# Optimization experiments

Hardware: AMD Instinct MI355X
Metric: run time of the kernel (lower is better)

## Reference

```python
import jax, jax.numpy as jnp
import numpy as np

B, T, N, F = 4, 24, 1024, 96
H, HD = 3, 32      # spatial GATConv: 3 heads, head-dim 32 (averaged -> 32 per branch, 3 branches -> 96)
GH, GHD = 4, 24    # GroupedGAT: 4 heads concatenated -> 96
E = 8192           # edges per graph


def setup_inputs() -> dict:
    key = jax.random.key(0)
    ks = jax.random.split(key, 24)
    s_in = 1.0 / np.sqrt(F)
    def gat_params(k):
        k1, k2, k3, k4 = jax.random.split(k, 4)
        return (jax.random.normal(k1, (F, H * HD), jnp.float32) * s_in,
                jax.random.normal(k2, (H, HD), jnp.float32) * 0.1,
                jax.random.normal(k3, (H, HD), jnp.float32) * 0.1,
                jax.random.normal(k4, (H, HD), jnp.float32) * 0.02)
    W_d, al_d, ar_d, b_d = gat_params(ks[3])
    W_m, al_m, ar_m, b_m = gat_params(ks[4])
    W_s, al_s, ar_s, b_s = gat_params(ks[5])
    inp = {
        "input": jax.random.normal(ks[0], (B, T, N, F), jnp.float32),
        "spatial_embedding": jax.random.normal(ks[1], (B, T, N, F), jnp.float32),
        "temporal_embedding": jax.random.normal(ks[2], (B, T, N, F), jnp.float32),
        "src_d": jax.random.randint(ks[6], (E,), 0, N, jnp.int32),
        "dst_d": (jnp.arange(E) % N).astype(jnp.int32),
        "src_m": jax.random.randint(ks[7], (E,), 0, N, jnp.int32),
        "dst_m": (jnp.arange(E) % N).astype(jnp.int32),
        "src_s": jax.random.randint(ks[8], (E,), 0, N, jnp.int32),
        "dst_s": (jnp.arange(E) % N).astype(jnp.int32),
        "W_d": W_d, "al_d": al_d, "ar_d": ar_d, "b_d": b_d,
        "W_m": W_m, "al_m": al_m, "ar_m": ar_m, "b_m": b_m,
        "W_s": W_s, "al_s": al_s, "ar_s": ar_s, "b_s": b_s,
        "Wg": jax.random.normal(ks[9], (F, GH * GHD), jnp.float32) * s_in,
        "agl": jax.random.normal(ks[10], (GH, GHD), jnp.float32) * 0.1,
        "agr": jax.random.normal(ks[11], (GH, GHD), jnp.float32) * 0.1,
        "Wf": jax.random.normal(ks[12], (2 * F, F), jnp.float32) * (1.0 / np.sqrt(2 * F)),
        "bf": jnp.zeros((F,), jnp.float32),
    }
    return inp


def _gat(x, src, dst, W, al, ar, b):
    # x: (N, K, F) node features with K = T*B batched feature slots
    K = x.shape[1]
    h = (x @ W).reshape(N, K, H, HD)                       # (N,K,H,HD)
    el = (h * al).sum(-1)                                  # (N,K,H)
    er = (h * ar).sum(-1)
    e = jax.nn.leaky_relu(el[src] + er[dst], 0.2)          # (E,K,H)
    emax = jax.ops.segment_max(e, dst, num_segments=N)
    emax = jnp.where(jnp.isfinite(emax), emax, 0.0)
    ex = jnp.exp(e - emax[dst])
    denom = jax.ops.segment_sum(ex, dst, num_segments=N)
    alpha = ex / (denom[dst] + 1e-9)                       # edge softmax over incoming edges
    out = jax.ops.segment_sum(h[src] * alpha[..., None], dst, num_segments=N)
    return (out + b).mean(2)                               # average heads -> (N,K,HD)


def reference(input, spatial_embedding, temporal_embedding,
              src_d, dst_d, src_m, dst_m, src_s, dst_s,
              W_d, al_d, ar_d, b_d, W_m, al_m, ar_m, b_m, W_s, al_s, ar_s, b_s,
              Wg, agl, agr, Wf, bf):
    # ---------------- SpatialBlock ----------------
    residual_s = input                                     # input_dim == output_dim
    x_in = input + spatial_embedding
    # torch: input.transpose(0,2).reshape(N,-1,F) -> slot order is (t,b)
    x = jnp.transpose(x_in, (2, 1, 0, 3)).reshape(N, T * B, F)
    xd = _gat(x, src_d, dst_d, W_d, al_d, ar_d, b_d)
    xm = _gat(x, src_m, dst_m, W_m, al_m, ar_m, b_m)
    xs = _gat(x, src_s, dst_s, W_s, al_s, ar_s, b_s)
    x_attn = jnp.concatenate([xd, xm, xs], axis=-1)        # (N, T*B, 3*HD=F)
    # torch: transpose(0,1).reshape(batch,T,N,-1)  (keeps original (t,b) slot order quirk)
    x_attn = jnp.transpose(x_attn, (1, 0, 2)).reshape(B, T, N, F)
    cov0 = spatial_embedding[:, 0]                         # (B,N,F)
    attn_S = jax.nn.softmax(cov0 @ jnp.swapaxes(cov0, 1, 2), axis=2)  # (B,N,N)
    # NOTE: embedding_x branch in SpatialBlock is dead code (out is overwritten); skipped.
    spatial = residual_s + x_attn

    # ---------------- TemporalBlock ----------------
    residual_t = input
    xt = jnp.swapaxes(input, 1, 2).reshape(B * N, T, F)    # (B*N, T, F), index k=b*N+n
    # GroupedGAT: dense multi-head GAT over the T=period_num time steps
    hg = (xt @ Wg).reshape(B * N, T, GH, GHD)
    elg = (hg * agl).sum(-1)                               # (BN,T,GH)
    erg = (hg * agr).sum(-1)
    eg = jax.nn.leaky_relu(elg[:, :, None, :] + erg[:, None, :, :], 0.2)  # (BN,Ti,Tj,GH)
    alphag = jax.nn.softmax(eg, axis=2)
    xg = jnp.einsum('kijh,kjhd->kihd', alphag, hg).reshape(B * N, T, GH * GHD)
    covT = temporal_embedding[:, :, 0]                     # (B,T,F)
    attn_T = jax.nn.softmax(covT @ jnp.swapaxes(covT, 1, 2), axis=1)      # softmax over dim=1 as in torch
    # torch: attn.repeat(N,1,1) paired with x of batch index b*N+n -> uses attn[(b*N+n) % B]
    idx = (jnp.arange(B * N) % B)
    emb = jnp.einsum('kij,kjf->kif', attn_T[idx], xt)      # (BN,T,F)
    xg = xg * jax.nn.sigmoid(emb)
    xg = jnp.swapaxes(xg.reshape(B, N, T, F), 1, 2)        # (B,T,N,F)
    temporal = residual_t + xg

    # ---------------- Fusion ----------------
    z = jax.nn.sigmoid(jnp.concatenate([spatial, temporal], axis=-1) @ Wf + bf)
    out = z * spatial + (1.0 - z) * temporal + input
    return out, attn_S
```

## Files before the change

kernel.cpp:

```cpp
#include <hip/hip_runtime.h>
#include <hip/hip_bf16.h>

typedef long long i64;
typedef __attribute__((ext_vector_type(8))) short short8b;
typedef __attribute__((ext_vector_type(4))) short short4b;
typedef __attribute__((ext_vector_type(4))) float f32x4;

union U8 { short8b v; ushort s[8]; };
union U4 { short4b v; ushort s[4]; };

static __device__ __forceinline__ float bs2f(ushort u) {
    union { unsigned int i; float f; } x; x.i = ((unsigned int)u) << 16; return x.f;
}
static __device__ __forceinline__ ushort f2bs(float f) {
    __hip_bfloat16 h = __float2bfloat16(f);
    return *reinterpret_cast<ushort*>(&h);
}
static __device__ __forceinline__ void mfma_bf16(f32x4& acc, short8b a, short8b b) {
    asm volatile("v_mfma_f32_16x16x32_bf16 %0, %1, %2, %0" : "+v"(acc) : "v"(a), "v"(b));
}
static __device__ __forceinline__ void mfma_fence() {
    asm volatile("s_nop 7\n\ts_nop 7\n\ts_nop 7");
}


__global__ __launch_bounds__(256) void prep_weights_kernel(
        const float* __restrict__ Wd, const float* __restrict__ Wm,
        const float* __restrict__ Ws, const float* __restrict__ Wg,
        const float* __restrict__ Wf,
        const float* __restrict__ ald, const float* __restrict__ ard,
        const float* __restrict__ alm, const float* __restrict__ arm,
        const float* __restrict__ als, const float* __restrict__ ars,
        const float* __restrict__ agl, const float* __restrict__ agr,
        ushort* __restrict__ wtab) {
    int idx = blockIdx.x * 256 + threadIdx.x;
    if (idx >= 61440) return;
    if (idx < 43008) {
        int w = idx / 10752, rem = idx - w * 10752;
        int c = rem / 96, k = rem - c * 96;
        float v;
        if (w < 3) {
            const float* W = (w == 0) ? Wd : (w == 1) ? Wm : Ws;
            if (c < 96) {
                v = W[k * 96 + c];
            } else {
                int j = c - 96, h = j >> 1;
                const float* a = (j & 1) ? ((w == 0) ? ard : (w == 1) ? arm : ars)
                                         : ((w == 0) ? ald : (w == 1) ? alm : als);
                v = 0.f;
                for (int d = 0; d < 32; ++d) v += W[k * 96 + h * 32 + d] * a[h * 32 + d];
            }
        } else {
            if (c < 96) {
                v = Wg[k * 96 + c];
            } else {
                int j = c - 96, g = j & 3;
                const float* a = (j >> 2) ? agr : agl;
                v = 0.f;
                for (int d = 0; d < 24; ++d) v += Wg[k * 96 + g * 24 + d] * a[g * 24 + d];
            }
        }
        wtab[w * 10752 + c * 96 + k] = f2bs(v);
    } else {
        int rem = idx - 43008;
        int c = rem / 192, k = rem - c * 192;
        wtab[43008 + c * 192 + k] = f2bs(Wf[k * 96 + c]);
    }
}

__global__ __launch_bounds__(256) void build_x_kernel(const float* __restrict__ inp,
                                                      const float* __restrict__ spat,
                                                      ushort* __restrict__ x) {
    int i4 = blockIdx.x * 256 + threadIdx.x;
    int q = i4 % 24;
    int r = i4 / 24;
    int n = r & 1023, bt = r >> 10;
    int t = bt % 24, b = bt / 24;
    int k = t * 4 + b;
    float4 a = ((const float4*)inp)[i4];
    float4 s = ((const float4*)spat)[i4];
    U4 u;
    u.s[0] = f2bs(a.x + s.x); u.s[1] = f2bs(a.y + s.y);
    u.s[2] = f2bs(a.z + s.z); u.s[3] = f2bs(a.w + s.w);
    *(short4b*)&x[((i64)((k << 10) | n)) * 96 + q * 4] = u.v;
}

__global__ __launch_bounds__(256) void gemm96_mfma_kernel(const ushort* __restrict__ X,
                                                          const ushort* __restrict__ wt,
                                                          ushort* __restrict__ Ho,
                                                          float* __restrict__ el,
                                                          float* __restrict__ er) {
    __shared__ ushort Xs[128 * 104];
    __shared__ ushort Wt[112 * 104];
    int tid = threadIdx.x;
    i64 row0 = (i64)blockIdx.x * 128;
    for (int i = tid; i < 1344; i += 256) {
        int c = i / 12, kg = i - c * 12;
        *(short8b*)&Wt[c * 104 + kg * 8] = *(const short8b*)&wt[c * 96 + kg * 8];
    }
    for (int i = tid; i < 1536; i += 256) {
        int r = i / 12, q = i - r * 12;
        *(short8b*)&Xs[r * 104 + q * 8] = *(const short8b*)&X[(row0 + r) * 96 + q * 8];
    }
    __syncthreads();
    int wid = tid >> 6, lane = tid & 63;
    int lr = lane & 15, lk = lane >> 4;
    f32x4 acc[2][7];
#pragma unroll
    for (int m = 0; m < 2; ++m)
#pragma unroll
        for (int c = 0; c < 7; ++c) acc[m][c] = (f32x4){0.f, 0.f, 0.f, 0.f};
    const ushort* xa = &Xs[(wid * 32 + lr) * 104 + lk * 8];
    const ushort* wb = &Wt[lr * 104 + lk * 8];
#pragma unroll
    for (int ks = 0; ks < 3; ++ks) {
        short8b a0 = *(const short8b*)(xa + ks * 32);
        short8b a1 = *(const short8b*)(xa + 16 * 104 + ks * 32);
#pragma unroll
        for (int c = 0; c < 7; ++c) {
            short8b b = *(const short8b*)(wb + c * 16 * 104 + ks * 32);
            mfma_bf16(acc[0][c], a0, b);
            mfma_bf16(acc[1][c], a1, b);
        }
    }
    mfma_fence();
#pragma unroll
    for (int m = 0; m < 2; ++m) {
#pragma unroll
        for (int c = 0; c < 6; ++c)
#pragma unroll
            for (int r = 0; r < 4; ++r) {
                i64 row = row0 + wid * 32 + m * 16 + lk * 4 + r;
                Ho[row * 96 + c * 16 + lr] = f2bs(acc[m][c][r]);
            }
        if (lr < 6) {
            float* dst = (lr & 1) ? er : el;
            int h = lr >> 1;
#pragma unroll
            for (int r = 0; r < 4; ++r) {
                i64 row = row0 + wid * 32 + m * 16 + lk * 4 + r;
                dst[row * 4 + h] = acc[m][6][r];
            }
        }
    }
}

__global__ __launch_bounds__(256) void gemm96_hg_mfma_kernel(const float* __restrict__ inp,
                                                             const ushort* __restrict__ wt,
                                                             ushort* __restrict__ Ho,
                                                             float* __restrict__ elg,
                                                             float* __restrict__ erg) {
    __shared__ ushort Xs[128 * 104];
    __shared__ ushort Wt[112 * 104];
    int tid = threadIdx.x;
    i64 row0 = (i64)blockIdx.x * 128;
    for (int i = tid; i < 1344; i += 256) {
        int c = i / 12, kg = i - c * 12;
        *(short8b*)&Wt[c * 104 + kg * 8] = *(const short8b*)&wt[c * 96 + kg * 8];
    }
    for (int i = tid; i < 3072; i += 256) {
        int r = i / 24, q = i - r * 24;
        int row = (int)row0 + r;
        int kk = row / 24, t = row - kk * 24;
        int b = kk >> 10, n = kk & 1023;
        float4 v = ((const float4*)inp)[((i64)(((b * 24 + t) << 10) | n)) * 24 + q];
        U4 u;
        u.s[0] = f2bs(v.x); u.s[1] = f2bs(v.y); u.s[2] = f2bs(v.z); u.s[3] = f2bs(v.w);
        *(short4b*)&Xs[r * 104 + q * 4] = u.v;
    }
    __syncthreads();
    int wid = tid >> 6, lane = tid & 63;
    int lr = lane & 15, lk = lane >> 4;
    f32x4 acc[2][7];
#pragma unroll
    for (int m = 0; m < 2; ++m)
#pragma unroll
        for (int c = 0; c < 7; ++c) acc[m][c] = (f32x4){0.f, 0.f, 0.f, 0.f};
    const ushort* xa = &Xs[(wid * 32 + lr) * 104 + lk * 8];
    const ushort* wb = &Wt[lr * 104 + lk * 8];
#pragma unroll
    for (int ks = 0; ks < 3; ++ks) {
        short8b a0 = *(const short8b*)(xa + ks * 32);
        short8b a1 = *(const short8b*)(xa + 16 * 104 + ks * 32);
#pragma unroll
        for (int c = 0; c < 7; ++c) {
            short8b b = *(const short8b*)(wb + c * 16 * 104 + ks * 32);
            mfma_bf16(acc[0][c], a0, b);
            mfma_bf16(acc[1][c], a1, b);
        }
    }
    mfma_fence();
#pragma unroll
    for (int m = 0; m < 2; ++m) {
#pragma unroll
        for (int c = 0; c < 6; ++c)
#pragma unroll
            for (int r = 0; r < 4; ++r) {
                i64 row = row0 + wid * 32 + m * 16 + lk * 4 + r;
                Ho[row * 96 + c * 16 + lr] = f2bs(acc[m][c][r]);
            }
        if (lr < 8) {
            float* dst = (lr >> 2) ? erg : elg;
            int g = lr & 3;
#pragma unroll
            for (int r = 0; r < 4; ++r) {
                i64 row = row0 + wid * 32 + m * 16 + lk * 4 + r;
                dst[row * 4 + g] = acc[m][6][r];
            }
        }
    }
}

__global__ __launch_bounds__(256) void gat_agg_kernel(const ushort* __restrict__ H2,
                                                      const float* __restrict__ el,
                                                      const float* __restrict__ er,
                                                      const int* __restrict__ src,
                                                      const float* __restrict__ bv,
                                                      ushort* __restrict__ xattn,
                                                      int g) {
    int tid = threadIdx.x;
    int pp = tid >> 3, l8 = tid & 7;
    int p = blockIdx.x * 32 + pp;
    int k = p >> 10, n = p & 1023;
    int d0 = l8 * 4;
    i64 kb = (i64)(k << 10);
    int s_own = src[n + l8 * 1024];
    float4 elv = *(const float4*)&el[(kb | s_own) * 4];
    float4 erv = *(const float4*)&er[(kb | n) * 4];
    float e[3], m[3];
    {
        float ev0 = elv.x + erv.x, ev1 = elv.y + erv.y, ev2 = elv.z + erv.z;
        e[0] = ev0 >= 0.f ? ev0 : 0.2f * ev0;
        e[1] = ev1 >= 0.f ? ev1 : 0.2f * ev1;
        e[2] = ev2 >= 0.f ? ev2 : 0.2f * ev2;
        m[0] = e[0]; m[1] = e[1]; m[2] = e[2];
    }
#pragma unroll
    for (int mask = 1; mask < 8; mask <<= 1) {
#pragma unroll
        for (int h = 0; h < 3; ++h) m[h] = fmaxf(m[h], __shfl_xor(m[h], mask, 8));
    }
    float pex[3], S[3];
#pragma unroll
    for (int h = 0; h < 3; ++h) { pex[h] = expf(e[h] - m[h]); S[h] = pex[h]; }
#pragma unroll
    for (int mask = 1; mask < 8; mask <<= 1) {
#pragma unroll
        for (int h = 0; h < 3; ++h) S[h] += __shfl_xor(S[h], mask, 8);
    }
    float w[3];
#pragma unroll
    for (int h = 0; h < 3; ++h) w[h] = pex[h] / (S[h] + 1e-9f);
    float acc[4] = {0.f, 0.f, 0.f, 0.f};
#pragma unroll
    for (int j = 0; j < 8; ++j) {
        int sj = __shfl(s_own, j, 8);
        float a0 = __shfl(w[0], j, 8);
        float a1 = __shfl(w[1], j, 8);
        float a2 = __shfl(w[2], j, 8);
        const ushort* hp = &H2[(kb | sj) * 96 + d0];
        U4 h0, h1, h2;
        h0.v = *(const short4b*)&hp[0];
        h1.v = *(const short4b*)&hp[32];
        h2.v = *(const short4b*)&hp[64];
#pragma unroll
        for (int c = 0; c < 4; ++c)
            acc[c] += a0 * bs2f(h0.s[c]) + a1 * bs2f(h1.s[c]) + a2 * bs2f(h2.s[c]);
    }
    float4 b0 = *(const float4*)&bv[d0];
    float4 b1 = *(const float4*)&bv[32 + d0];
    float4 b2 = *(const float4*)&bv[64 + d0];
    float bsum[4] = {b0.x + b1.x + b2.x, b0.y + b1.y + b2.y,
                     b0.z + b1.z + b2.z, b0.w + b1.w + b2.w};
    U4 u;
#pragma unroll
    for (int c = 0; c < 4; ++c) u.s[c] = f2bs((acc[c] + bsum[c]) * (1.f / 3.f));
    *(short4b*)&xattn[(kb | n) * 96 + g * 32 + d0] = u.v;
}

__global__ __launch_bounds__(256) void attn_scores_kernel(const float* __restrict__ spat,
                                                          float* __restrict__ attnS) {
    extern __shared__ __align__(16) float dynf[];
    float* As = dynf;
    float* Bs = dynf + 12800;
    int bid = blockIdx.x;
    int b = bid >> 7;
    int it = (bid >> 4) & 7;
    int jt = bid & 15;
    int i0 = it * 128, j0 = jt * 64;
    const float* C = spat + (i64)b * 24 * 1024 * 96;
    int tid = threadIdx.x;
    float4* As4 = (float4*)As;
    float4* Bs4 = (float4*)Bs;
    const float4* Ai = (const float4*)(C + (i64)i0 * 96);
    const float4* Bj = (const float4*)(C + (i64)j0 * 96);
    for (int i = tid; i < 3072; i += 256) {
        int row = i / 24, q = i - row * 24;
        As4[row * 25 + q] = Ai[i];
    }
    for (int i = tid; i < 1536; i += 256) {
        int row = i / 24, q = i - row * 24;
        Bs4[row * 25 + q] = Bj[i];
    }
    __syncthreads();
    int tj = tid & 15, ti = tid >> 4;
    float acc[8][4];
#pragma unroll
    for (int r = 0; r < 8; ++r)
#pragma unroll
        for (int s = 0; s < 4; ++s) acc[r][s] = 0.f;
    for (int k4 = 0; k4 < 24; ++k4) {
        float4 a[8], bv[4];
#pragma unroll
        for (int r = 0; r < 8; ++r) a[r] = As4[(ti * 8 + r) * 25 + k4];
#pragma unroll
        for (int s = 0; s < 4; ++s) bv[s] = Bs4[(s * 16 + tj) * 25 + k4];
#pragma unroll
        for (int r = 0; r < 8; ++r)
#pragma unroll
            for (int s = 0; s < 4; ++s)
                acc[r][s] += a[r].x * bv[s].x + a[r].y * bv[s].y + a[r].z * bv[s].z + a[r].w * bv[s].w;
    }
#pragma unroll
    for (int r = 0; r < 8; ++r) {
        i64 orow = ((i64)(b << 10) + i0 + ti * 8 + r) * 1024 + j0;
#pragma unroll
        for (int s = 0; s < 4; ++s) attnS[orow + s * 16 + tj] = acc[r][s];
    }
}

__global__ __launch_bounds__(256) void attn_softmax_kernel(float* __restrict__ attnS) {
    i64 base = (i64)blockIdx.x * 1024;
    float4* row4 = (float4*)(attnS + base);
    int tid = threadIdx.x;
    float4 v = row4[tid];
    __shared__ float red[256];
    float m = fmaxf(fmaxf(v.x, v.y), fmaxf(v.z, v.w));
    red[tid] = m;
    __syncthreads();
    for (int st = 128; st > 0; st >>= 1) {
        if (tid < st) red[tid] = fmaxf(red[tid], red[tid + st]);
        __syncthreads();
    }
    m = red[0];
    __syncthreads();
    v.x = expf(v.x - m); v.y = expf(v.y - m); v.z = expf(v.z - m); v.w = expf(v.w - m);
    red[tid] = v.x + v.y + v.z + v.w;
    __syncthreads();
    for (int st = 128; st > 0; st >>= 1) {
        if (tid < st) red[tid] += red[tid + st];
        __syncthreads();
    }
    float inv = 1.f / red[0];
    v.x *= inv; v.y *= inv; v.z *= inv; v.w *= inv;
    row4[tid] = v;
}

__global__ __launch_bounds__(576) void attn_t_kernel(const float* __restrict__ temp,
                                                     float* __restrict__ attnT) {
    int b = blockIdx.x;
    int tid = threadIdx.x;
    __shared__ float cs[24][96];
    __shared__ float M[24][24];
    for (int i = tid; i < 2304; i += 576) {
        int r = i / 96, f = i - r * 96;
        cs[r][f] = temp[((i64)(b * 24 + r)) * 1024 * 96 + f];
    }
    __syncthreads();
    int i = tid / 24, j = tid - i * 24;
    float s = 0.f;
#pragma unroll
    for (int f = 0; f < 96; ++f) s += cs[i][f] * cs[j][f];
    M[i][j] = s;
    __syncthreads();
    float m = -1e30f;
#pragma unroll
    for (int i2 = 0; i2 < 24; ++i2) m = fmaxf(m, M[i2][j]);
    float sum = 0.f;
#pragma unroll
    for (int i2 = 0; i2 < 24; ++i2) sum += expf(M[i2][j] - m);
    attnT[((i64)b * 24 + i) * 24 + j] = expf(M[i][j] - m) / sum;
}

__global__ __launch_bounds__(576) void sig_kernel(const float* __restrict__ inp,
                                                  const float* __restrict__ attnT,
                                                  ushort* __restrict__ sig) {
    int kk = blockIdx.x;
    int b = kk >> 10, n = kk & 1023;
    __shared__ __align__(16) float xs[24 * 100];
    __shared__ float ats[576];
    int tid = threadIdx.x;
    {
        int r = tid / 24, q = tid - (tid / 24) * 24;
        *(float4*)&xs[r * 100 + q * 4] =
            ((const float4*)inp)[(((i64)(b * 24 + r)) << 10 | n) * 24 + q];
        ats[tid] = attnT[(kk & 3) * 576 + tid];
    }
    __syncthreads();
    int i = tid / 24, f4 = tid - (tid / 24) * 24;
    const float* ap = &ats[i * 24];
    float4 acc = {0.f, 0.f, 0.f, 0.f};
#pragma unroll
    for (int j = 0; j < 24; ++j) {
        float a = ap[j];
        float4 v = *(const float4*)&xs[j * 100 + f4 * 4];
        acc.x += a * v.x; acc.y += a * v.y; acc.z += a * v.z; acc.w += a * v.w;
    }
    U4 o;
    o.s[0] = f2bs(1.f / (1.f + expf(-acc.x)));
    o.s[1] = f2bs(1.f / (1.f + expf(-acc.y)));
    o.s[2] = f2bs(1.f / (1.f + expf(-acc.z)));
    o.s[3] = f2bs(1.f / (1.f + expf(-acc.w)));
    *(short4b*)&sig[(i64)kk * 2304 + i * 96 + f4 * 4] = o.v;
}

__global__ __launch_bounds__(192) void xg_kernel(const ushort* __restrict__ hg,
                                                 const float* __restrict__ elgb,
                                                 const float* __restrict__ ergb,
                                                 const ushort* __restrict__ sig,
                                                 ushort* __restrict__ gated) {
    int kk = blockIdx.x;
    __shared__ __align__(16) ushort hgs[24 * 96];
    __shared__ __align__(16) float alphaT[4 * 24 * 32];
    __shared__ __align__(16) float elg[24][4], erg[24][4];
    int tid = threadIdx.x;
    for (int i = tid; i < 576; i += 192)
        *(short4b*)&hgs[i * 4] = *(const short4b*)&hg[(i64)kk * 2304 + i * 4];
    for (int i = tid; i < 48; i += 192) {
        int r = i >> 1;
        if (i & 1) *(float4*)&erg[r][0] = ((const float4*)ergb)[(i64)kk * 24 + r];
        else       *(float4*)&elg[r][0] = ((const float4*)elgb)[(i64)kk * 24 + r];
    }
    __syncthreads();
    {
        int i = tid >> 3, g = (tid >> 1) & 3, half = tid & 1;
        int j0 = half * 12;
        float eli = elg[i][g];
        float ev[12];
        float m = -1e30f;
#pragma unroll
        for (int j = 0; j < 12; ++j) {
            float e = eli + erg[j0 + j][g];
            e = e >= 0.f ? e : 0.2f * e;
            ev[j] = e;
            m = fmaxf(m, e);
        }
        m = fmaxf(m, __shfl_xor(m, 1));
        float sum = 0.f;
#pragma unroll
        for (int j = 0; j < 12; ++j) { ev[j] = expf(ev[j] - m); sum += ev[j]; }
        sum += __shfl_xor(sum, 1);
        float inv = 1.f / sum;
        int slot = ((i / 3) * 4 + (i - (i / 3) * 3)) ^ (g << 3);
#pragma unroll
        for (int j = 0; j < 12; ++j) alphaT[g * 768 + (j0 + j) * 32 + slot] = ev[j] * inv;
    }
    __syncthreads();
    int ig = tid / 24, f4 = tid - (tid / 24) * 24;
    int g = f4 / 6;
    float4 xg0 = {0,0,0,0}, xg1 = {0,0,0,0}, xg2 = {0,0,0,0};
    const float* aT = &alphaT[g * 768 + ((ig * 4) ^ (g << 3))];
#pragma unroll
    for (int j = 0; j < 24; ++j) {
        U4 uh; uh.v = *(const short4b*)&hgs[j * 96 + f4 * 4];
        float4 a4 = *(const float4*)&aT[j * 32];
        float h0 = bs2f(uh.s[0]), h1 = bs2f(uh.s[1]), h2 = bs2f(uh.s[2]), h3 = bs2f(uh.s[3]);
        xg0.x += a4.x * h0; xg0.y += a4.x * h1; xg0.z += a4.x * h2; xg0.w += a4.x * h3;
        xg1.x += a4.y * h0; xg1.y += a4.y * h1; xg1.z += a4.y * h2; xg1.w += a4.y * h3;
        xg2.x += a4.z * h0; xg2.y += a4.z * h1; xg2.z += a4.z * h2; xg2.w += a4.z * h3;
    }
    i64 obase = (i64)kk * 2304 + f4 * 4;
#pragma unroll
    for (int r = 0; r < 3; ++r) {
        float4 xg = (r == 0) ? xg0 : (r == 1) ? xg1 : xg2;
        i64 off = obase + (i64)(ig * 3 + r) * 96;
        U4 us; us.v = *(const short4b*)&sig[off];
        U4 o;
        o.s[0] = f2bs(xg.x * bs2f(us.s[0]));
        o.s[1] = f2bs(xg.y * bs2f(us.s[1]));
        o.s[2] = f2bs(xg.z * bs2f(us.s[2]));
        o.s[3] = f2bs(xg.w * bs2f(us.s[3]));
        *(short4b*)&gated[off] = o.v;
    }
}

__global__ __launch_bounds__(384) void fusion_mfma_kernel(const float* __restrict__ inp,
                                                          const ushort* __restrict__ xattn,
                                                          const ushort* __restrict__ gated,
                                                          const ushort* __restrict__ wtf,
                                                          const float* __restrict__ bfv,
                                                          float* __restrict__ outb) {
    extern __shared__ __align__(16) ushort dynlds[];
    ushort* Xs = dynlds;
    ushort* Wt = dynlds + 96 * 200;
    float* zbuf = (float*)Wt;
    int tid = threadIdx.x;
    i64 row0 = (i64)blockIdx.x * 96;
    for (int i = tid; i < 2304; i += 384) {
        int c = i / 24, kg = i - c * 24;
        *(short8b*)&Wt[c * 200 + kg * 8] = *(const short8b*)&wtf[c * 192 + kg * 8];
    }
    for (int i = tid; i < 1152; i += 384) {
        int r = i / 12, q = i - r * 12;
        i64 grow = row0 + r;
        int n = (int)(grow & 1023);
        int bt = (int)(grow >> 10);
        int t = bt % 24, b = bt / 24;
        float4 iv0 = ((const float4*)inp)[grow * 24 + q * 2];
        float4 iv1 = ((const float4*)inp)[grow * 24 + q * 2 + 1];
        U8 xa; xa.v = *(const short8b*)&xattn[grow * 96 + q * 8];
        U8 gd; gd.v = *(const short8b*)&gated[(((i64)((b << 10) | n)) * 24 + t) * 96 + q * 8];
        float ivf[8] = {iv0.x, iv0.y, iv0.z, iv0.w, iv1.x, iv1.y, iv1.z, iv1.w};
        U8 sp, tm;
#pragma unroll
        for (int j = 0; j < 8; ++j) {
            sp.s[j] = f2bs(ivf[j] + bs2f(xa.s[j]));
            tm.s[j] = f2bs(ivf[j] + bs2f(gd.s[j]));
        }
        *(short8b*)&Xs[r * 200 + q * 8] = sp.v;
        *(short8b*)&Xs[r * 200 + 96 + q * 8] = tm.v;
    }
    __syncthreads();
    int wid = tid >> 6, lane = tid & 63;
    int lr = lane & 15, lk = lane >> 4;
    f32x4 acc[6];
#pragma unroll
    for (int c = 0; c < 6; ++c) acc[c] = (f32x4){0.f, 0.f, 0.f, 0.f};
    const ushort* xa = &Xs[(wid * 16 + lr) * 200 + lk * 8];
    const ushort* wb = &Wt[lr * 200 + lk * 8];
#pragma unroll
    for (int ks = 0; ks < 6; ++ks) {
        short8b a = *(const short8b*)(xa + ks * 32);
#pragma unroll
        for (int c = 0; c < 6; ++c) {
            short8b b = *(const short8b*)(wb + c * 16 * 200 + ks * 32);
            mfma_bf16(acc[c], a, b);
        }
    }
    mfma_fence();
    float4 ivp[6];
#pragma unroll
    for (int ii = 0; ii < 6; ++ii) {
        int i = tid + ii * 384;
        int r2 = i / 24, q = i - r2 * 24;
        ivp[ii] = ((const float4*)inp)[(row0 + r2) * 24 + q];
    }
    __syncthreads();
#pragma unroll
    for (int c = 0; c < 6; ++c) {
        int col = c * 16 + lr;
        float bfc = bfv[col];
#pragma unroll
        for (int r = 0; r < 4; ++r) {
            int lrow = wid * 16 + lk * 4 + r;
            zbuf[lrow * 100 + col] = 1.f / (1.f + expf(-(acc[c][r] + bfc)));
        }
    }
    __syncthreads();
#pragma unroll
    for (int ii = 0; ii < 6; ++ii) {
        int i = tid + ii * 384;
        int r2 = i / 24, q = i - r2 * 24;
        i64 grow = row0 + r2;
        float4 iv = ivp[ii];
        float4 zv = *(const float4*)&zbuf[r2 * 100 + q * 4];
        U4 spv; spv.v = *(const short4b*)&Xs[r2 * 200 + q * 4];
        U4 tmv; tmv.v = *(const short4b*)&Xs[r2 * 200 + 96 + q * 4];
        float4 o;
        o.x = zv.x * bs2f(spv.s[0]) + (1.f - zv.x) * bs2f(tmv.s[0]) + iv.x;
        o.y = zv.y * bs2f(spv.s[1]) + (1.f - zv.y) * bs2f(tmv.s[1]) + iv.y;
        o.z = zv.z * bs2f(spv.s[2]) + (1.f - zv.z) * bs2f(tmv.s[2]) + iv.z;
        o.w = zv.w * bs2f(spv.s[3]) + (1.f - zv.w) * bs2f(tmv.s[3]) + iv.w;
        ((float4*)outb)[grow * 24 + q] = o;
    }
}

extern "C" void kernel_launch(void* const* d_in, const int* in_sizes, int n_in,
                              void* d_out, int out_size, void* d_ws, size_t ws_size,
                              hipStream_t stream) {
    const float* input = (const float*)d_in[0];
    const float* spat  = (const float*)d_in[1];
    const float* temp  = (const float*)d_in[2];
    const int* src_d = (const int*)d_in[3];
    const int* src_m = (const int*)d_in[5];
    const int* src_s = (const int*)d_in[7];
    const float* W_d  = (const float*)d_in[9];
    const float* al_d = (const float*)d_in[10];
    const float* ar_d = (const float*)d_in[11];
    const float* b_d  = (const float*)d_in[12];
    const float* W_m  = (const float*)d_in[13];
    const float* al_m = (const float*)d_in[14];
    const float* ar_m = (const float*)d_in[15];
    const float* b_m  = (const float*)d_in[16];
    const float* W_s  = (const float*)d_in[17];
    const float* al_s = (const float*)d_in[18];
    const float* ar_s = (const float*)d_in[19];
    const float* b_s  = (const float*)d_in[20];
    const float* Wg   = (const float*)d_in[21];
    const float* agl  = (const float*)d_in[22];
    const float* agr  = (const float*)d_in[23];
    const float* Wf   = (const float*)d_in[24];
    const float* bf_  = (const float*)d_in[25];

    float* outb  = (float*)d_out;
    float* attnS = outb + 9437184;

    float* wsf = (float*)d_ws;
    ushort* xbf      = (ushort*)wsf;
    ushort* hgbf     = xbf;
    ushort* H2bf     = (ushort*)(wsf + 4718592);
    ushort* gatedbf  = H2bf;
    ushort* xattnbf  = (ushort*)(wsf + 9437184);
    float* el    = wsf + 14155776;
    float* er    = wsf + 14548992;
    float* elgb  = el;
    float* ergb  = er;
    ushort* wtab = (ushort*)(wsf + 14942208);
    ushort* wt_d = wtab;
    ushort* wt_m = wtab + 10752;
    ushort* wt_s = wtab + 21504;
    ushort* wtg  = wtab + 32256;
    ushort* wtf  = wtab + 43008;
    float* attnT = wsf + 14972928;
    ushort* sigbf = (ushort*)outb;

    static int attr_set = 0;
    if (!attr_set) {
        hipFuncSetAttribute((const void*)fusion_mfma_kernel,
                            hipFuncAttributeMaxDynamicSharedMemorySize, 76800);
        hipFuncSetAttribute((const void*)attn_scores_kernel,
                            hipFuncAttributeMaxDynamicSharedMemorySize, 76800);
        attr_set = 1;
    }

    prep_weights_kernel<<<240, 256, 0, stream>>>(W_d, W_m, W_s, Wg, Wf,
                                                 al_d, ar_d, al_m, ar_m, al_s, ar_s,
                                                 agl, agr, wtab);
    build_x_kernel<<<9216, 256, 0, stream>>>(input, spat, xbf);

    const ushort* Wgat[3] = {wt_d, wt_m, wt_s};
    const float* bgat[3] = {b_d, b_m, b_s};
    const int* srcs[3] = {src_d, src_m, src_s};
    for (int g = 0; g < 3; ++g) {
        gemm96_mfma_kernel<<<768, 256, 0, stream>>>(xbf, Wgat[g], H2bf, el, er);
        gat_agg_kernel<<<3072, 256, 0, stream>>>(H2bf, el, er, srcs[g], bgat[g],
                                                 xattnbf, g);
    }

    attn_scores_kernel<<<512, 256, 76800, stream>>>(spat, attnS);
    attn_softmax_kernel<<<4096, 256, 0, stream>>>(attnS);

    attn_t_kernel<<<4, 576, 0, stream>>>(temp, attnT);
    sig_kernel<<<4096, 576, 0, stream>>>(input, attnT, sigbf);
    gemm96_hg_mfma_kernel<<<768, 256, 0, stream>>>(input, wtg, hgbf, elgb, ergb);
    xg_kernel<<<4096, 192, 0, stream>>>(hgbf, elgb, ergb, sigbf, gatedbf);
    fusion_mfma_kernel<<<1024, 384, 76800, stream>>>(input, xattnbf, gatedbf, wtf,
                                                     bf_, outb);
}
```

Measured before the change: 251.7 us.

## Fuse build_x into GAT GEMMs and merge sigmoid gate into xg kernel

Removes the build_x kernel: each of the three spatial GEMM launches now reads input and spatial_embedding in fp32, adds them and converts to bf16 while staging its tile in shared memory. The sig and xg kernels become a single 576-thread kernel that computes the temporal-attention sigmoid gate in registers, so the bf16 sig buffer no longer makes a round trip through memory. The fusion kernel also stops prefetching the input residual into registers before the matmul and instead loads it in the epilogue. The trade-off is that the input+spatial add and conversion is now redone in each of the three GEMM launches, which read fp32 data twice per launch.

```diff
diff --git a/kernel.cpp b/kernel.cpp
--- a/kernel.cpp
+++ b/kernel.cpp
@@ -68,24 +68,8 @@
     }
 }
 
-__global__ __launch_bounds__(256) void build_x_kernel(const float* __restrict__ inp,
-                                                      const float* __restrict__ spat,
-                                                      ushort* __restrict__ x) {
-    int i4 = blockIdx.x * 256 + threadIdx.x;
-    int q = i4 % 24;
-    int r = i4 / 24;
-    int n = r & 1023, bt = r >> 10;
-    int t = bt % 24, b = bt / 24;
-    int k = t * 4 + b;
-    float4 a = ((const float4*)inp)[i4];
-    float4 s = ((const float4*)spat)[i4];
-    U4 u;
-    u.s[0] = f2bs(a.x + s.x); u.s[1] = f2bs(a.y + s.y);
-    u.s[2] = f2bs(a.z + s.z); u.s[3] = f2bs(a.w + s.w);
-    *(short4b*)&x[((i64)((k << 10) | n)) * 96 + q * 4] = u.v;
-}
-
-__global__ __launch_bounds__(256) void gemm96_mfma_kernel(const ushort* __restrict__ X,
+__global__ __launch_bounds__(256) void gemm96_mfma_kernel(const float* __restrict__ inp,
+                                                          const float* __restrict__ spat,
                                                           const ushort* __restrict__ wt,
                                                           ushort* __restrict__ Ho,
                                                           float* __restrict__ el,
@@ -98,9 +82,18 @@
         int c = i / 12, kg = i - c * 12;
         *(short8b*)&Wt[c * 104 + kg * 8] = *(const short8b*)&wt[c * 96 + kg * 8];
     }
-    for (int i = tid; i < 1536; i += 256) {
-        int r = i / 12, q = i - r * 12;
-        *(short8b*)&Xs[r * 104 + q * 8] = *(const short8b*)&X[(row0 + r) * 96 + q * 8];
+    for (int i = tid; i < 3072; i += 256) {
+        int r = i / 24, q = i - r * 24;
+        int row = (int)row0 + r;
+        int k = row >> 10, n = row & 1023;
+        int bb = k & 3, t = k >> 2;
+        i64 base = ((i64)(((bb * 24 + t) << 10) | n)) * 24 + q;
+        float4 a = ((const float4*)inp)[base];
+        float4 s = ((const float4*)spat)[base];
+        U4 u;
+        u.s[0] = f2bs(a.x + s.x); u.s[1] = f2bs(a.y + s.y);
+        u.s[2] = f2bs(a.z + s.z); u.s[3] = f2bs(a.w + s.w);
+        *(short4b*)&Xs[r * 104 + q * 4] = u.v;
     }
     __syncthreads();
     int wid = tid >> 6, lane = tid & 63;
@@ -382,57 +375,32 @@
     attnT[((i64)b * 24 + i) * 24 + j] = expf(M[i][j] - m) / sum;
 }
 
-__global__ __launch_bounds__(576) void sig_kernel(const float* __restrict__ inp,
-                                                  const float* __restrict__ attnT,
-                                                  ushort* __restrict__ sig) {
+__global__ __launch_bounds__(576) void sigxg_kernel(const float* __restrict__ inp,
+                                                    const float* __restrict__ attnT,
+                                                    const ushort* __restrict__ hg,
+                                                    const float* __restrict__ elgb,
+                                                    const float* __restrict__ ergb,
+                                                    ushort* __restrict__ gated) {
     int kk = blockIdx.x;
     int b = kk >> 10, n = kk & 1023;
     __shared__ __align__(16) float xs[24 * 100];
     __shared__ float ats[576];
-    int tid = threadIdx.x;
-    {
-        int r = tid / 24, q = tid - (tid / 24) * 24;
-        *(float4*)&xs[r * 100 + q * 4] =
-            ((const float4*)inp)[(((i64)(b * 24 + r)) << 10 | n) * 24 + q];
-        ats[tid] = attnT[(kk & 3) * 576 + tid];
-    }
-    __syncthreads();
-    int i = tid / 24, f4 = tid - (tid / 24) * 24;
-    const float* ap = &ats[i * 24];
-    float4 acc = {0.f, 0.f, 0.f, 0.f};
-#pragma unroll
-    for (int j = 0; j < 24; ++j) {
-        float a = ap[j];
-        float4 v = *(const float4*)&xs[j * 100 + f4 * 4];
-        acc.x += a * v.x; acc.y += a * v.y; acc.z += a * v.z; acc.w += a * v.w;
-    }
-    U4 o;
-    o.s[0] = f2bs(1.f / (1.f + expf(-acc.x)));
-    o.s[1] = f2bs(1.f / (1.f + expf(-acc.y)));
-    o.s[2] = f2bs(1.f / (1.f + expf(-acc.z)));
-    o.s[3] = f2bs(1.f / (1.f + expf(-acc.w)));
-    *(short4b*)&sig[(i64)kk * 2304 + i * 96 + f4 * 4] = o.v;
-}
-
-__global__ __launch_bounds__(192) void xg_kernel(const ushort* __restrict__ hg,
-                                                 const float* __restrict__ elgb,
-                                                 const float* __restrict__ ergb,
-                                                 const ushort* __restrict__ sig,
-                                                 ushort* __restrict__ gated) {
-    int kk = blockIdx.x;
     __shared__ __align__(16) ushort hgs[24 * 96];
     __shared__ __align__(16) float alphaT[4 * 24 * 32];
     __shared__ __align__(16) float elg[24][4], erg[24][4];
     int tid = threadIdx.x;
-    for (int i = tid; i < 576; i += 192)
-        *(short4b*)&hgs[i * 4] = *(const short4b*)&hg[(i64)kk * 2304 + i * 4];
-    for (int i = tid; i < 48; i += 192) {
-        int r = i >> 1;
-        if (i & 1) *(float4*)&erg[r][0] = ((const float4*)ergb)[(i64)kk * 24 + r];
-        else       *(float4*)&elg[r][0] = ((const float4*)elgb)[(i64)kk * 24 + r];
-    }
-    __syncthreads();
-    {
+    int r = tid / 24, q = tid - r * 24;
+    ((float4*)xs)[r * 25 + q] =
+        ((const float4*)inp)[(((i64)(b * 24 + r)) << 10 | n) * 24 + q];
+    ats[tid] = attnT[(kk & 3) * 576 + tid];
+    *(short4b*)&hgs[tid * 4] = *(const short4b*)&hg[(i64)kk * 2304 + tid * 4];
+    if (tid < 48) {
+        int rr = tid >> 1;
+        if (tid & 1) *(float4*)&erg[rr][0] = ((const float4*)ergb)[(i64)kk * 24 + rr];
+        else         *(float4*)&elg[rr][0] = ((const float4*)elgb)[(i64)kk * 24 + rr];
+    }
+    __syncthreads();
+    if (tid < 192) {
         int i = tid >> 3, g = (tid >> 1) & 3, half = tid & 1;
         int j0 = half * 12;
         float eli = elg[i][g];
@@ -455,33 +423,38 @@
 #pragma unroll
         for (int j = 0; j < 12; ++j) alphaT[g * 768 + (j0 + j) * 32 + slot] = ev[j] * inv;
     }
-    __syncthreads();
-    int ig = tid / 24, f4 = tid - (tid / 24) * 24;
-    int g = f4 / 6;
-    float4 xg0 = {0,0,0,0}, xg1 = {0,0,0,0}, xg2 = {0,0,0,0};
-    const float* aT = &alphaT[g * 768 + ((ig * 4) ^ (g << 3))];
+    float4 emb = {0.f, 0.f, 0.f, 0.f};
+    {
+        const float* ap = &ats[r * 24];
+#pragma unroll
+        for (int j = 0; j < 24; ++j) {
+            float a = ap[j];
+            float4 v = *(const float4*)&xs[j * 100 + q * 4];
+            emb.x += a * v.x; emb.y += a * v.y; emb.z += a * v.z; emb.w += a * v.w;
+        }
+    }
+    float sg0 = 1.f / (1.f + expf(-emb.x));
+    float sg1 = 1.f / (1.f + expf(-emb.y));
+    float sg2 = 1.f / (1.f + expf(-emb.z));
+    float sg3 = 1.f / (1.f + expf(-emb.w));
+    __syncthreads();
+    int g = q / 6;
+    int slot = ((r / 3) * 4 + (r - (r / 3) * 3)) ^ (g << 3);
+    const float* aT = &alphaT[g * 768 + slot];
+    float4 xg = {0.f, 0.f, 0.f, 0.f};
 #pragma unroll
     for (int j = 0; j < 24; ++j) {
-        U4 uh; uh.v = *(const short4b*)&hgs[j * 96 + f4 * 4];
-        float4 a4 = *(const float4*)&aT[j * 32];
-        float h0 = bs2f(uh.s[0]), h1 = bs2f(uh.s[1]), h2 = bs2f(uh.s[2]), h3 = bs2f(uh.s[3]);
-        xg0.x += a4.x * h0; xg0.y += a4.x * h1; xg0.z += a4.x * h2; xg0.w += a4.x * h3;
-        xg1.x += a4.y * h0; xg1.y += a4.y * h1; xg1.z += a4.y * h2; xg1.w += a4.y * h3;
-        xg2.x += a4.z * h0; xg2.y += a4.z * h1; xg2.z += a4.z * h2; xg2.w += a4.z * h3;
-    }
-    i64 obase = (i64)kk * 2304 + f4 * 4;
-#pragma unroll
-    for (int r = 0; r < 3; ++r) {
-        float4 xg = (r == 0) ? xg0 : (r == 1) ? xg1 : xg2;
-        i64 off = obase + (i64)(ig * 3 + r) * 96;
-        U4 us; us.v = *(const short4b*)&sig[off];
-        U4 o;
-        o.s[0] = f2bs(xg.x * bs2f(us.s[0]));
-        o.s[1] = f2bs(xg.y * bs2f(us.s[1]));
-        o.s[2] = f2bs(xg.z * bs2f(us.s[2]));
-        o.s[3] = f2bs(xg.w * bs2f(us.s[3]));
-        *(short4b*)&gated[off] = o.v;
-    }
+        float a = aT[j * 32];
+        U4 uh; uh.v = *(const short4b*)&hgs[j * 96 + q * 4];
+        xg.x += a * bs2f(uh.s[0]); xg.y += a * bs2f(uh.s[1]);
+        xg.z += a * bs2f(uh.s[2]); xg.w += a * bs2f(uh.s[3]);
+    }
+    U4 o;
+    o.s[0] = f2bs(xg.x * sg0);
+    o.s[1] = f2bs(xg.y * sg1);
+    o.s[2] = f2bs(xg.z * sg2);
+    o.s[3] = f2bs(xg.w * sg3);
+    *(short4b*)&gated[(i64)kk * 2304 + r * 96 + q * 4] = o.v;
 }
 
 __global__ __launch_bounds__(384) void fusion_mfma_kernel(const float* __restrict__ inp,
@@ -538,13 +511,6 @@
         }
     }
     mfma_fence();
-    float4 ivp[6];
-#pragma unroll
-    for (int ii = 0; ii < 6; ++ii) {
-        int i = tid + ii * 384;
-        int r2 = i / 24, q = i - r2 * 24;
-        ivp[ii] = ((const float4*)inp)[(row0 + r2) * 24 + q];
-    }
     __syncthreads();
 #pragma unroll
     for (int c = 0; c < 6; ++c) {
@@ -557,12 +523,10 @@
         }
     }
     __syncthreads();
-#pragma unroll
-    for (int ii = 0; ii < 6; ++ii) {
-        int i = tid + ii * 384;
+    for (int i = tid; i < 2304; i += 384) {
         int r2 = i / 24, q = i - r2 * 24;
         i64 grow = row0 + r2;
-        float4 iv = ivp[ii];
+        float4 iv = ((const float4*)inp)[grow * 24 + q];
         float4 zv = *(const float4*)&zbuf[r2 * 100 + q * 4];
         U4 spv; spv.v = *(const short4b*)&Xs[r2 * 200 + q * 4];
         U4 tmv; tmv.v = *(const short4b*)&Xs[r2 * 200 + 96 + q * 4];
@@ -606,8 +570,7 @@
     float* attnS = outb + 9437184;
 
     float* wsf = (float*)d_ws;
-    ushort* xbf      = (ushort*)wsf;
-    ushort* hgbf     = xbf;
+    ushort* hgbf     = (ushort*)wsf;
     ushort* H2bf     = (ushort*)(wsf + 4718592);
     ushort* gatedbf  = H2bf;
     ushort* xattnbf  = (ushort*)(wsf + 9437184);
@@ -622,7 +585,6 @@
     ushort* wtg  = wtab + 32256;
     ushort* wtf  = wtab + 43008;
     float* attnT = wsf + 14972928;
-    ushort* sigbf = (ushort*)outb;
 
     static int attr_set = 0;
     if (!attr_set) {
@@ -636,13 +598,12 @@
     prep_weights_kernel<<<240, 256, 0, stream>>>(W_d, W_m, W_s, Wg, Wf,
                                                  al_d, ar_d, al_m, ar_m, al_s, ar_s,
                                                  agl, agr, wtab);
-    build_x_kernel<<<9216, 256, 0, stream>>>(input, spat, xbf);
 
     const ushort* Wgat[3] = {wt_d, wt_m, wt_s};
     const float* bgat[3] = {b_d, b_m, b_s};
     const int* srcs[3] = {src_d, src_m, src_s};
     for (int g = 0; g < 3; ++g) {
-        gemm96_mfma_kernel<<<768, 256, 0, stream>>>(xbf, Wgat[g], H2bf, el, er);
+        gemm96_mfma_kernel<<<768, 256, 0, stream>>>(input, spat, Wgat[g], H2bf, el, er);
         gat_agg_kernel<<<3072, 256, 0, stream>>>(H2bf, el, er, srcs[g], bgat[g],
                                                  xattnbf, g);
     }
@@ -651,9 +612,8 @@
     attn_softmax_kernel<<<4096, 256, 0, stream>>>(attnS);
 
     attn_t_kernel<<<4, 576, 0, stream>>>(temp, attnT);
-    sig_kernel<<<4096, 576, 0, stream>>>(input, attnT, sigbf);
     gemm96_hg_mfma_kernel<<<768, 256, 0, stream>>>(input, wtg, hgbf, elgb, ergb);
-    xg_kernel<<<4096, 192, 0, stream>>>(hgbf, elgb, ergb, sigbf, gatedbf);
+    sigxg_kernel<<<4096, 576, 0, stream>>>(input, attnT, hgbf, elgb, ergb, gatedbf);
     fusion_mfma_kernel<<<1024, 384, 76800, stream>>>(input, xattnbf, gatedbf, wtf,
                                                      bf_, outb);
 }
```

Measured after the change: 256.3 us. No clear change (+1.8%).
